# Kernel tuning notes

Hardware: AMD Instinct MI355X
Metric: run time of the kernel (lower is better)

The kernel has to match this reference:

```python
import jax, jax.numpy as jnp
import numpy as np

EPS = 1e-5          # InstanceNorm2d default eps
SLOPE = 0.01        # LeakyReLU default negative_slope
C = 256


def setup_inputs() -> dict:
    key = jax.random.key(0)
    k = jax.random.split(key, 5)
    B, H, W = 8, 128, 128
    x = jax.random.normal(k[0], (B, C, H, W), dtype=jnp.float32)
    # attn: Conv2d(C, C//4, 1, bias=False) then Conv2d(C//4, C, 1, bias=False)
    attn_w1 = jax.random.normal(k[1], (C // 4, C), dtype=jnp.float32) * (1.0 / np.sqrt(C))
    attn_w2 = jax.random.normal(k[2], (C, C // 4), dtype=jnp.float32) * (1.0 / np.sqrt(C // 4))
    # refine: depthwise Conv2d(C, C, 3, padding=1, groups=C) with bias
    refine_w = jax.random.normal(k[3], (C, 1, 3, 3), dtype=jnp.float32) * (1.0 / 3.0)
    refine_b = jax.random.normal(k[4], (C,), dtype=jnp.float32) * 0.01
    return {"x": x, "attn_w1": attn_w1, "attn_w2": attn_w2,
            "refine_w": refine_w, "refine_b": refine_b}


def reference(x, attn_w1, attn_w2, refine_w, refine_b):
    # The torch module runs pywt wavedec2 -> waverec2 on x[b,c].detach().
    # With db2 (symmetric mode) and H,W divisible by 2^level, waverec2 is a
    # perfect-reconstruction identity and interpolate to (H,W) is a no-op,
    # so x_wave == stop_gradient(x) exactly.
    xw = jax.lax.stop_gradient(x)

    # --- channel attention (squeeze-excite with 1x1 convs == GEMMs) ---
    p = jnp.mean(xw, axis=(2, 3))                      # [B, C] global avg pool
    h = jax.nn.leaky_relu(p @ attn_w1.T, SLOPE)        # [B, C//4]
    a = jax.nn.sigmoid(h @ attn_w2.T)                  # [B, C]
    y = xw * a[:, :, None, None]

    # --- depthwise 3x3 refine conv ---
    y = jax.lax.conv_general_dilated(
        y, refine_w, window_strides=(1, 1), padding='SAME',
        feature_group_count=C,
        dimension_numbers=('NCHW', 'OIHW', 'NCHW'))
    y = y + refine_b[None, :, None, None]

    # --- InstanceNorm2d (affine=False, biased variance) ---
    mu = jnp.mean(y, axis=(2, 3), keepdims=True)
    var = jnp.mean(jnp.square(y - mu), axis=(2, 3), keepdims=True)
    y = (y - mu) * jax.lax.rsqrt(var + EPS)

    return jax.nn.leaky_relu(y, SLOPE)
```

## Files before the change

kernel.cpp:

```cpp
#include <hip/hip_runtime.h>
#include <hip/hip_bf16.h>
#include <math.h>

#define NPLANE 2048
#define HW     16384
#define HH     128
#define WW     128
#define SLOPE  0.01f
#define EPS    1e-5f

__global__ __launch_bounds__(256) void k_plane_mean(const float* __restrict__ x,
                                                    float* __restrict__ p) {
    const int plane = blockIdx.x;
    const float4* x4 = (const float4*)(x + (size_t)plane * HW);
    float s = 0.f;
#pragma unroll
    for (int i = 0; i < 16; ++i) {
        float4 v = x4[i * 256 + threadIdx.x];
        s += (v.x + v.y) + (v.z + v.w);
    }
#pragma unroll
    for (int off = 32; off; off >>= 1) s += __shfl_down(s, off, 64);
    __shared__ float red[4];
    const int wave = threadIdx.x >> 6, lane = threadIdx.x & 63;
    if (lane == 0) red[wave] = s;
    __syncthreads();
    if (threadIdx.x == 0) {
        float t = (red[0] + red[1]) + (red[2] + red[3]);
        p[plane] = t * (1.f / (float)HW);
    }
}

__global__ __launch_bounds__(256) void k_attn(const float* __restrict__ p,
                                              const float* __restrict__ w1,
                                              const float* __restrict__ w2,
                                              float* __restrict__ a) {
    __shared__ float ps[NPLANE];
    __shared__ float hs[512];
    for (int i = threadIdx.x; i < NPLANE; i += 256) ps[i] = p[i];
    __syncthreads();
    for (int t = threadIdx.x; t < 512; t += 256) {
        const int b = t >> 6, j = t & 63;
        const float* prow = ps + b * 256;
        const float* wrow = w1 + j * 256;
        float acc = 0.f;
#pragma unroll 8
        for (int k = 0; k < 256; ++k) acc += prow[k] * wrow[k];
        hs[b * 64 + j] = acc > 0.f ? acc : SLOPE * acc;
    }
    __syncthreads();
    for (int t = threadIdx.x; t < NPLANE; t += 256) {
        const int b = t >> 8, c = t & 255;
        const float* hrow = hs + b * 64;
        const float* wrow = w2 + c * 64;
        float acc = 0.f;
#pragma unroll 8
        for (int k = 0; k < 64; ++k) acc += hrow[k] * wrow[k];
        a[t] = 1.f / (1.f + __expf(-acc));
    }
}

__global__ __launch_bounds__(256) void k_main(const float* __restrict__ x,
                                              const float* __restrict__ rw,
                                              const float* __restrict__ rb,
                                              const float* __restrict__ a,
                                              float* __restrict__ out) {
    __shared__ float tile[HW];
    const int plane = blockIdx.x;
    const int ch = plane & 255;

    {
        const float4* x4 = (const float4*)(x + (size_t)plane * HW);
        float4* t4 = (float4*)tile;
#pragma unroll
        for (int i = 0; i < 16; ++i) t4[i * 256 + threadIdx.x] = x4[i * 256 + threadIdx.x];
    }

    float w0 = rw[ch * 9 + 0], w1 = rw[ch * 9 + 1], w2 = rw[ch * 9 + 2];
    float w3 = rw[ch * 9 + 3], w4 = rw[ch * 9 + 4], w5 = rw[ch * 9 + 5];
    float w6 = rw[ch * 9 + 6], w7 = rw[ch * 9 + 7], w8 = rw[ch * 9 + 8];
    const float bias = rb[ch];
    const float av = a[plane];

    __syncthreads();

    const int c = threadIdx.x & 127;
    const int r0 = (threadIdx.x >> 7) * 64;

    float l0, m0, q0, l1, m1, q1, l2, m2, q2;

#define LOADROW(row, L, M, Q)                                         \
    do {                                                              \
        int _r = (row);                                               \
        if (_r < 0 || _r > 127) { L = 0.f; M = 0.f; Q = 0.f; }        \
        else {                                                        \
            const float* rp = tile + _r * WW;                         \
            M = rp[c];                                                \
            L = (c > 0)   ? rp[c - 1] : 0.f;                          \
            Q = (c < 127) ? rp[c + 1] : 0.f;                          \
        }                                                             \
    } while (0)

    LOADROW(r0 - 1, l0, m0, q0);
    LOADROW(r0,     l1, m1, q1);

    float y[64];
    float s = 0.f, sq = 0.f;
#pragma unroll
    for (int j = 0; j < 64; ++j) {
        LOADROW(r0 + j + 1, l2, m2, q2);
        float conv = w0 * l0 + w1 * m0 + w2 * q0
                   + w3 * l1 + w4 * m1 + w5 * q1
                   + w6 * l2 + w7 * m2 + w8 * q2;
        float v = conv * av + bias;
        y[j] = v;
        s += v;
        sq += v * v;
        l0 = l1; m0 = m1; q0 = q1;
        l1 = l2; m1 = m2; q1 = q2;
    }
#undef LOADROW

#pragma unroll
    for (int off = 32; off; off >>= 1) {
        s  += __shfl_down(s,  off, 64);
        sq += __shfl_down(sq, off, 64);
    }
    __syncthreads();
    const int wave = threadIdx.x >> 6, lane = threadIdx.x & 63;
    if (lane == 0) { tile[wave] = s; tile[4 + wave] = sq; }
    __syncthreads();
    const float S  = (tile[0] + tile[1]) + (tile[2] + tile[3]);
    const float SQ = (tile[4] + tile[5]) + (tile[6] + tile[7]);
    const float mean = S * (1.f / (float)HW);
    const float var  = SQ * (1.f / (float)HW) - mean * mean;
    const float rstd = rsqrtf(var + EPS);

    float* op = out + (size_t)plane * HW;
#pragma unroll
    for (int j = 0; j < 64; ++j) {
        float v = (y[j] - mean) * rstd;
        v = v > 0.f ? v : SLOPE * v;
        op[(r0 + j) * WW + c] = v;
    }
}

extern "C" void kernel_launch(void* const* d_in, const int* in_sizes, int n_in,
                              void* d_out, int out_size, void* d_ws, size_t ws_size,
                              hipStream_t stream) {
    const float* x  = (const float*)d_in[0];
    const float* w1 = (const float*)d_in[1];
    const float* w2 = (const float*)d_in[2];
    const float* rw = (const float*)d_in[3];
    const float* rb = (const float*)d_in[4];
    float* out = (float*)d_out;

    float* p = (float*)d_ws;
    float* a = p + NPLANE;

    k_plane_mean<<<NPLANE, 256, 0, stream>>>(x, p);
    k_attn<<<1, 256, 0, stream>>>(p, w1, w2, a);
    k_main<<<NPLANE, 256, 0, stream>>>(x, rw, rb, a, out);
}
```

Baseline: 299.2 us.

## Fuse attention into main kernel, drop LDS tile, recompute conv from global

Removes the single-block attention kernel and has every main block recompute its own hidden vector and sigmoid gate from the pooled means. The 64KB LDS plane tile and the 64-element register array are dropped. The depthwise conv is computed twice, once for statistics and once for output, reading x straight from global/L2. Bias is dropped and the gate is folded into the normalisation scale algebraically, since the instance norm cancels both. This raises occupancy and removes a serial launch, but adds a second pass over x and redundant per-block GEMV work.

Result: slower. 307.7 us (+2.8%).

```diff
diff --git a/kernel.cpp b/kernel.cpp
--- a/kernel.cpp
+++ b/kernel.cpp
@@ -4,7 +4,6 @@
 
 #define NPLANE 2048
 #define HW     16384
-#define HH     128
 #define WW     128
 #define SLOPE  0.01f
 #define EPS    1e-5f
@@ -31,118 +30,110 @@
     }
 }
 
-__global__ __launch_bounds__(256) void k_attn(const float* __restrict__ p,
+__global__ __launch_bounds__(256) void k_main(const float* __restrict__ x,
                                               const float* __restrict__ w1,
                                               const float* __restrict__ w2,
-                                              float* __restrict__ a) {
-    __shared__ float ps[NPLANE];
-    __shared__ float hs[512];
-    for (int i = threadIdx.x; i < NPLANE; i += 256) ps[i] = p[i];
-    __syncthreads();
-    for (int t = threadIdx.x; t < 512; t += 256) {
-        const int b = t >> 6, j = t & 63;
-        const float* prow = ps + b * 256;
-        const float* wrow = w1 + j * 256;
-        float acc = 0.f;
-#pragma unroll 8
-        for (int k = 0; k < 256; ++k) acc += prow[k] * wrow[k];
-        hs[b * 64 + j] = acc > 0.f ? acc : SLOPE * acc;
-    }
-    __syncthreads();
-    for (int t = threadIdx.x; t < NPLANE; t += 256) {
-        const int b = t >> 8, c = t & 255;
-        const float* hrow = hs + b * 64;
-        const float* wrow = w2 + c * 64;
-        float acc = 0.f;
-#pragma unroll 8
-        for (int k = 0; k < 64; ++k) acc += hrow[k] * wrow[k];
-        a[t] = 1.f / (1.f + __expf(-acc));
-    }
-}
+                                              const float* __restrict__ rw,
+                                              const float* __restrict__ p,
+                                              float* __restrict__ out) {
+    __shared__ float hs[64];
+    __shared__ float red[8];
+    __shared__ float sh_a;
 
-__global__ __launch_bounds__(256) void k_main(const float* __restrict__ x,
-                                              const float* __restrict__ rw,
-                                              const float* __restrict__ rb,
-                                              const float* __restrict__ a,
-                                              float* __restrict__ out) {
-    __shared__ float tile[HW];
     const int plane = blockIdx.x;
+    const int b = plane >> 8;
     const int ch = plane & 255;
 
     {
-        const float4* x4 = (const float4*)(x + (size_t)plane * HW);
-        float4* t4 = (float4*)tile;
+        const int j = threadIdx.x >> 2;
+        const int part = threadIdx.x & 3;
+        const float4* pr = (const float4*)(p + b * 256 + part * 64);
+        const float4* wr = (const float4*)(w1 + j * 256 + part * 64);
+        float acc = 0.f;
 #pragma unroll
-        for (int i = 0; i < 16; ++i) t4[i * 256 + threadIdx.x] = x4[i * 256 + threadIdx.x];
+        for (int k = 0; k < 16; ++k) {
+            float4 pv = pr[k], wv = wr[k];
+            acc += pv.x * wv.x + pv.y * wv.y + pv.z * wv.z + pv.w * wv.w;
+        }
+        acc += __shfl_xor(acc, 1, 64);
+        acc += __shfl_xor(acc, 2, 64);
+        if (part == 0) hs[j] = acc > 0.f ? acc : SLOPE * acc;
+    }
+    __syncthreads();
+    if (threadIdx.x < 64) {
+        float v = w2[ch * 64 + threadIdx.x] * hs[threadIdx.x];
+#pragma unroll
+        for (int off = 32; off; off >>= 1) v += __shfl_down(v, off, 64);
+        if (threadIdx.x == 0) sh_a = 1.f / (1.f + expf(-v));
     }
 
-    float w0 = rw[ch * 9 + 0], w1 = rw[ch * 9 + 1], w2 = rw[ch * 9 + 2];
-    float w3 = rw[ch * 9 + 3], w4 = rw[ch * 9 + 4], w5 = rw[ch * 9 + 5];
-    float w6 = rw[ch * 9 + 6], w7 = rw[ch * 9 + 7], w8 = rw[ch * 9 + 8];
-    const float bias = rb[ch];
-    const float av = a[plane];
+    const float w_0 = rw[ch * 9 + 0], w_1 = rw[ch * 9 + 1], w_2 = rw[ch * 9 + 2];
+    const float w_3 = rw[ch * 9 + 3], w_4 = rw[ch * 9 + 4], w_5 = rw[ch * 9 + 5];
+    const float w_6 = rw[ch * 9 + 6], w_7 = rw[ch * 9 + 7], w_8 = rw[ch * 9 + 8];
 
-    __syncthreads();
-
+    const float* xp = x + (size_t)plane * HW;
     const int c = threadIdx.x & 127;
     const int r0 = (threadIdx.x >> 7) * 64;
 
-    float l0, m0, q0, l1, m1, q1, l2, m2, q2;
-
-#define LOADROW(row, L, M, Q)                                         \
-    do {                                                              \
-        int _r = (row);                                               \
-        if (_r < 0 || _r > 127) { L = 0.f; M = 0.f; Q = 0.f; }        \
-        else {                                                        \
-            const float* rp = tile + _r * WW;                         \
-            M = rp[c];                                                \
-            L = (c > 0)   ? rp[c - 1] : 0.f;                          \
-            Q = (c < 127) ? rp[c + 1] : 0.f;                          \
-        }                                                             \
+#define LOADROW(row, L, M, Q)                                          \
+    do {                                                               \
+        const int _r = (row);                                          \
+        if (_r >= 0 && _r <= 127) {                                    \
+            const float* rp = xp + _r * WW;                            \
+            M = rp[c];                                                 \
+            L = (c > 0)   ? rp[c - 1] : 0.f;                           \
+            Q = (c < 127) ? rp[c + 1] : 0.f;                           \
+        } else { L = 0.f; M = 0.f; Q = 0.f; }                          \
     } while (0)
 
+#define CONV9() (w_0 * l0 + w_1 * m0 + w_2 * q0                        \
+               + w_3 * l1 + w_4 * m1 + w_5 * q1                        \
+               + w_6 * l2 + w_7 * m2 + w_8 * q2)
+
+    float l0, m0, q0, l1, m1, q1, l2, m2, q2;
     LOADROW(r0 - 1, l0, m0, q0);
     LOADROW(r0,     l1, m1, q1);
-
-    float y[64];
     float s = 0.f, sq = 0.f;
-#pragma unroll
+#pragma unroll 8
     for (int j = 0; j < 64; ++j) {
         LOADROW(r0 + j + 1, l2, m2, q2);
-        float conv = w0 * l0 + w1 * m0 + w2 * q0
-                   + w3 * l1 + w4 * m1 + w5 * q1
-                   + w6 * l2 + w7 * m2 + w8 * q2;
-        float v = conv * av + bias;
-        y[j] = v;
-        s += v;
-        sq += v * v;
+        const float conv = CONV9();
+        s += conv;
+        sq += conv * conv;
         l0 = l1; m0 = m1; q0 = q1;
         l1 = l2; m1 = m2; q1 = q2;
     }
-#undef LOADROW
 
 #pragma unroll
     for (int off = 32; off; off >>= 1) {
         s  += __shfl_down(s,  off, 64);
         sq += __shfl_down(sq, off, 64);
     }
+    const int wave = threadIdx.x >> 6, lane = threadIdx.x & 63;
+    if (lane == 0) { red[wave] = s; red[4 + wave] = sq; }
     __syncthreads();
-    const int wave = threadIdx.x >> 6, lane = threadIdx.x & 63;
-    if (lane == 0) { tile[wave] = s; tile[4 + wave] = sq; }
-    __syncthreads();
-    const float S  = (tile[0] + tile[1]) + (tile[2] + tile[3]);
-    const float SQ = (tile[4] + tile[5]) + (tile[6] + tile[7]);
-    const float mean = S * (1.f / (float)HW);
-    const float var  = SQ * (1.f / (float)HW) - mean * mean;
-    const float rstd = rsqrtf(var + EPS);
+    const float S  = (red[0] + red[1]) + (red[2] + red[3]);
+    const float SQ = (red[4] + red[5]) + (red[6] + red[7]);
+    const float mean_c = S * (1.f / (float)HW);
+    const float var_c  = SQ * (1.f / (float)HW) - mean_c * mean_c;
+    const float a      = sh_a;
+    const float scale  = a * rsqrtf(a * a * var_c + EPS);
 
     float* op = out + (size_t)plane * HW;
-#pragma unroll
+    LOADROW(r0 - 1, l0, m0, q0);
+    LOADROW(r0,     l1, m1, q1);
+#pragma unroll 8
     for (int j = 0; j < 64; ++j) {
-        float v = (y[j] - mean) * rstd;
+        LOADROW(r0 + j + 1, l2, m2, q2);
+        const float conv = CONV9();
+        float v = scale * (conv - mean_c);
         v = v > 0.f ? v : SLOPE * v;
         op[(r0 + j) * WW + c] = v;
+        l0 = l1; m0 = m1; q0 = q1;
+        l1 = l2; m1 = m2; q1 = q2;
     }
+#undef LOADROW
+#undef CONV9
 }
 
 extern "C" void kernel_launch(void* const* d_in, const int* in_sizes, int n_in,
@@ -152,13 +143,10 @@
     const float* w1 = (const float*)d_in[1];
     const float* w2 = (const float*)d_in[2];
     const float* rw = (const float*)d_in[3];
-    const float* rb = (const float*)d_in[4];
     float* out = (float*)d_out;
 
     float* p = (float*)d_ws;
-    float* a = p + NPLANE;
 
     k_plane_mean<<<NPLANE, 256, 0, stream>>>(x, p);
-    k_attn<<<1, 256, 0, stream>>>(p, w1, w2, a);
-    k_main<<<NPLANE, 256, 0, stream>>>(x, rw, rb, a, out);
+    k_main<<<NPLANE, 256, 0, stream>>>(x, w1, w2, rw, p, out);
 }
```
